# Performance work log

Measured on AMD Instinct MI355X. Metric: run time of the kernel, lower is better.

Reference implementation:

```python
import jax, jax.numpy as jnp
import numpy as np

N_EXPERTS = 8
D_MODEL = 1024
D_FF = 2048
NUM_TOKENS = 16384


def setup_inputs() -> dict:
    key = jax.random.key(0)
    k1, k2, k3, k4 = jax.random.split(key, 4)
    x = jax.random.normal(k1, (NUM_TOKENS, D_MODEL), dtype=jnp.float32)
    expert_indices = jax.random.randint(k2, (NUM_TOKENS,), 0, N_EXPERTS, dtype=jnp.int32)
    # init per nn.init.normal_(std=0.02)
    gate_up_weight = 0.02 * jax.random.normal(k3, (N_EXPERTS, 2 * D_FF, D_MODEL), dtype=jnp.float32)
    down_weight = 0.02 * jax.random.normal(k4, (N_EXPERTS, D_MODEL, D_FF), dtype=jnp.float32)
    return {"x": x, "expert_indices": expert_indices,
            "gate_up_weight": gate_up_weight, "down_weight": down_weight}


def reference(x, expert_indices, gate_up_weight, down_weight):
    # Faithful math: each token t uses expert e = expert_indices[t]:
    #   combined = x @ gate_up_weight[e].T ; gate, up = split ; h = silu(gate)*up
    #   out = h @ down_weight[e].T
    # Implemented as a fixed loop over the (small) expert set with masked
    # accumulation, avoiding the original's per-token [2F,D] weight gather.
    n_experts = gate_up_weight.shape[0]
    d_ff = down_weight.shape[2]
    out = jnp.zeros((x.shape[0], down_weight.shape[1]), dtype=x.dtype)
    for e in range(n_experts):
        combined = x @ gate_up_weight[e].T                  # [T, 2*d_ff]
        gate, up = combined[:, :d_ff], combined[:, d_ff:]
        hidden = jax.nn.silu(gate) * up                     # [T, d_ff]
        o = hidden @ down_weight[e].T                       # [T, d_model]
        out = out + jnp.where((expert_indices == e)[:, None], o, 0.0)
    return out
```

## Files before the change

### kernel.cpp

```cpp
#include <hip/hip_runtime.h>

#define NTOK 16384
#define DM 1024
#define DFF 2048
#define NE 8

typedef unsigned short u16;
typedef __attribute__((ext_vector_type(8))) short bf16x8;
typedef __attribute__((ext_vector_type(4))) float f32x4;

__device__ __forceinline__ u16 f2bf(float f) {
  unsigned u = __float_as_uint(f);
  u += 0x7fff + ((u >> 16) & 1);
  return (u16)(u >> 16);
}

__device__ __forceinline__ void async16(const void* g, void* l) {
  __builtin_amdgcn_global_load_lds(
      (const __attribute__((address_space(1))) unsigned int*)g,
      (__attribute__((address_space(3))) unsigned int*)l, 16, 0, 0);
}

__global__ void k_count(const int* __restrict__ idx, int* __restrict__ counts) {
  int t = blockIdx.x * 256 + threadIdx.x;
  atomicAdd(&counts[idx[t]], 1);
}

__global__ void k_offsets(int* __restrict__ c) {
  if (threadIdx.x == 0) {
    int acc = 0;
    for (int e = 0; e < NE; e++) { c[8 + e] = acc; c[16 + e] = acc; acc += c[e]; }
  }
}

__global__ void k_scatter(const int* __restrict__ idx, int* __restrict__ cursor,
                          int* __restrict__ tl) {
  int t = blockIdx.x * 256 + threadIdx.x;
  int pos = atomicAdd(&cursor[idx[t]], 1);
  tl[pos] = t;
}

__global__ void k_cvt_xw(const float* __restrict__ x, const float* __restrict__ wgu,
                         u16* __restrict__ xb, u16* __restrict__ wgub) {
  const size_t N1 = (size_t)NTOK * DM;
  const size_t N2 = (size_t)NE * 2 * DFF * DM;
  const size_t total4 = (N1 + N2) / 4;
  for (size_t q = (size_t)blockIdx.x * 256 + threadIdx.x; q < total4;
       q += (size_t)gridDim.x * 256) {
    size_t i = q * 4;
    const float* s;
    u16* d;
    if (i < N1) { s = x + i; d = xb + i; }
    else { s = wgu + (i - N1); d = wgub + (i - N1); }
    float4 v = *(const float4*)s;
    ushort4 o;
    o.x = f2bf(v.x); o.y = f2bf(v.y); o.z = f2bf(v.z); o.w = f2bf(v.w);
    *(ushort4*)d = o;
  }
}

__global__ __launch_bounds__(512, 2) void k_gemm1(
    const u16* __restrict__ xb, const u16* __restrict__ wgu,
    u16* __restrict__ hid, const int* __restrict__ tl,
    const int* __restrict__ offs, const int* __restrict__ counts,
    const float* __restrict__ wd, u16* __restrict__ wdb) {
  int wg = blockIdx.x;
  int tid = threadIdx.x;

  {
    const size_t WD4 = (size_t)NE * DM * DFF / 4;
    for (size_t i = (size_t)wg * 512 + tid; i < WD4; i += (size_t)1152 * 512) {
      float4 v = *(const float4*)(wd + i * 4);
      ushort4 o;
      o.x = f2bf(v.x); o.y = f2bf(v.y); o.z = f2bf(v.z); o.w = f2bf(v.w);
      *(ushort4*)(wdb + i * 4) = o;
    }
  }

  int e = wg & 7;
  int r = wg >> 3;
  int bx = r % 9;
  int by = r / 9;
  int Me = counts[e];
  int m0 = bx * 256;
  if (m0 >= Me) return;
  int n0 = by * 128;
  int oe = offs[e];
  const int* tle = tl + oe;

  int lane = tid & 63;
  int wid = tid >> 6;
  int wm = wid >> 2;
  int wn = wid & 3;

  __shared__ u16 lds[2][2][256 * 64];

  int lr = lane >> 3;
  int swz = ((lane & 7) ^ lr) * 8;
  const u16* pA[4];
  const u16* pB[4];
#pragma unroll
  for (int j = 0; j < 4; j++) {
    int c = j * 8 + wid;
    int a = m0 + c * 8 + lr;
    if (a >= Me) a = Me - 1;
    pA[j] = xb + (size_t)tle[a] * DM + swz;
    int b = c * 8 + lr;
    int grow = ((b >> 5) & 1) * DFF + n0 + ((b >> 6) & 3) * 32 + (b & 31);
    pB[j] = wgu + ((size_t)e * 2 * DFF + grow) * DM + swz;
  }

  f32x4 acc[8][4];
#pragma unroll
  for (int m = 0; m < 8; m++)
#pragma unroll
    for (int f = 0; f < 4; f++) acc[m][f] = (f32x4){0.f, 0.f, 0.f, 0.f};

  const int r15 = lane & 15;
  const int hi4 = lane >> 4;
  const int rx = r15 & 7;

#pragma unroll
  for (int j = 0; j < 4; j++) {
    int off = (j * 8 + wid) * 1024;
    async16(pA[j], (char*)&lds[0][0][0] + off);
    async16(pB[j], (char*)&lds[0][1][0] + off);
  }
  asm volatile("s_waitcnt vmcnt(0)" ::: "memory");
  __builtin_amdgcn_s_barrier();
  __builtin_amdgcn_sched_barrier(0);

  int cur = 0;
#pragma unroll 1
  for (int t = 0; t < DM / 64; t++) {
    const char* Ab = (const char*)&lds[cur][0][0];
    const char* Bb = (const char*)&lds[cur][1][0];
    char* LA = (char*)&lds[cur ^ 1][0][0];
    char* LB = (char*)&lds[cur ^ 1][1][0];
    int k1 = (t + 1) * 64;
    bool pf = (t < DM / 64 - 1);
    bf16x8 bfr[4][2];
#pragma unroll
    for (int p = 0; p < 4; p++) {
      if (p == 0) {
#pragma unroll
        for (int f = 0; f < 4; f++)
#pragma unroll
          for (int kk = 0; kk < 2; kk++) {
            int row = wn * 64 + f * 16 + r15;
            bfr[f][kk] = *(const bf16x8*)(Bb + row * 128 + (((kk * 4 + hi4) ^ rx) * 16));
          }
      }
      bf16x8 af[2][2];
#pragma unroll
      for (int i = 0; i < 2; i++)
#pragma unroll
        for (int kk = 0; kk < 2; kk++) {
          int row = wm * 128 + (2 * p + i) * 16 + r15;
          af[i][kk] = *(const bf16x8*)(Ab + row * 128 + (((kk * 4 + hi4) ^ rx) * 16));
        }
      if (pf && p < 2) {
#pragma unroll
        for (int j = 0; j < 2; j++) {
          int jj = p * 2 + j;
          int off = (jj * 8 + wid) * 1024;
          async16(pA[jj] + k1, LA + off);
          async16(pB[jj] + k1, LB + off);
        }
      }
      __builtin_amdgcn_sched_barrier(0);
      __builtin_amdgcn_s_setprio(1);
#pragma unroll
      for (int kk = 0; kk < 2; kk++)
#pragma unroll
        for (int i = 0; i < 2; i++)
#pragma unroll
          for (int f = 0; f < 4; f++)
            acc[2 * p + i][f] = __builtin_amdgcn_mfma_f32_16x16x32_bf16(
                af[i][kk], bfr[f][kk], acc[2 * p + i][f], 0, 0, 0);
      __builtin_amdgcn_s_setprio(0);
      __builtin_amdgcn_sched_barrier(0);
    }
    asm volatile("s_waitcnt vmcnt(0)" ::: "memory");
    __builtin_amdgcn_s_barrier();
    __builtin_amdgcn_sched_barrier(0);
    cur ^= 1;
  }

  int colb = n0 + wn * 32 + r15;
#pragma unroll
  for (int m = 0; m < 8; m++) {
#pragma unroll
    for (int rr = 0; rr < 4; rr++) {
      int gm = m0 + wm * 128 + m * 16 + hi4 * 4 + rr;
      if (gm < Me) {
        size_t rowp = (size_t)(oe + gm) * DFF;
#pragma unroll
        for (int f = 0; f < 2; f++) {
          float g = acc[m][f][rr];
          float u = acc[m][f + 2][rr];
          float s = g / (1.0f + __expf(-g));
          hid[rowp + colb + f * 16] = f2bf(s * u);
        }
      }
    }
  }
}

__global__ __launch_bounds__(512, 2) void k_gemm2(
    const u16* __restrict__ hid, const u16* __restrict__ wd,
    float* __restrict__ out, const int* __restrict__ tl,
    const int* __restrict__ offs, const int* __restrict__ counts) {
  int wg = blockIdx.x;
  int e = wg & 7;
  int r = wg >> 3;
  int bx = r % 9;
  int by = r / 9;
  int Me = counts[e];
  int m0 = bx * 256;
  if (m0 >= Me) return;
  int n0 = by * 256;
  int oe = offs[e];
  const int* tle = tl + oe;

  int tid = threadIdx.x;
  int lane = tid & 63;
  int wid = tid >> 6;
  int wm = wid >> 2;
  int wn = wid & 3;

  __shared__ u16 lds[2][2][256 * 64];

  int lr = lane >> 3;
  int swz = ((lane & 7) ^ lr) * 8;
  const u16* pA[4];
  const u16* pB[4];
#pragma unroll
  for (int j = 0; j < 4; j++) {
    int c = j * 8 + wid;
    int a = m0 + c * 8 + lr;
    if (a >= Me) a = Me - 1;
    pA[j] = hid + (size_t)(oe + a) * DFF + swz;
    pB[j] = wd + ((size_t)e * DM + n0 + c * 8 + lr) * DFF + swz;
  }

  f32x4 acc[8][4];
#pragma unroll
  for (int m = 0; m < 8; m++)
#pragma unroll
    for (int f = 0; f < 4; f++) acc[m][f] = (f32x4){0.f, 0.f, 0.f, 0.f};

  const int r15 = lane & 15;
  const int hi4 = lane >> 4;
  const int rx = r15 & 7;

#pragma unroll
  for (int j = 0; j < 4; j++) {
    int off = (j * 8 + wid) * 1024;
    async16(pA[j], (char*)&lds[0][0][0] + off);
    async16(pB[j], (char*)&lds[0][1][0] + off);
  }
  asm volatile("s_waitcnt vmcnt(0)" ::: "memory");
  __builtin_amdgcn_s_barrier();
  __builtin_amdgcn_sched_barrier(0);

  int cur = 0;
#pragma unroll 1
  for (int t = 0; t < DFF / 64; t++) {
    const char* Ab = (const char*)&lds[cur][0][0];
    const char* Bb = (const char*)&lds[cur][1][0];
    char* LA = (char*)&lds[cur ^ 1][0][0];
    char* LB = (char*)&lds[cur ^ 1][1][0];
    int k1 = (t + 1) * 64;
    bool pf = (t < DFF / 64 - 1);
    bf16x8 bfr[4][2];
#pragma unroll
    for (int p = 0; p < 4; p++) {
      if (p == 0) {
#pragma unroll
        for (int f = 0; f < 4; f++)
#pragma unroll
          for (int kk = 0; kk < 2; kk++) {
            int row = wn * 64 + f * 16 + r15;
            bfr[f][kk] = *(const bf16x8*)(Bb + row * 128 + (((kk * 4 + hi4) ^ rx) * 16));
          }
      }
      bf16x8 af[2][2];
#pragma unroll
      for (int i = 0; i < 2; i++)
#pragma unroll
        for (int kk = 0; kk < 2; kk++) {
          int row = wm * 128 + (2 * p + i) * 16 + r15;
          af[i][kk] = *(const bf16x8*)(Ab + row * 128 + (((kk * 4 + hi4) ^ rx) * 16));
        }
      if (pf && p < 2) {
#pragma unroll
        for (int j = 0; j < 2; j++) {
          int jj = p * 2 + j;
          int off = (jj * 8 + wid) * 1024;
          async16(pA[jj] + k1, LA + off);
          async16(pB[jj] + k1, LB + off);
        }
      }
      __builtin_amdgcn_sched_barrier(0);
      __builtin_amdgcn_s_setprio(1);
#pragma unroll
      for (int kk = 0; kk < 2; kk++)
#pragma unroll
        for (int i = 0; i < 2; i++)
#pragma unroll
          for (int f = 0; f < 4; f++)
            acc[2 * p + i][f] = __builtin_amdgcn_mfma_f32_16x16x32_bf16(
                af[i][kk], bfr[f][kk], acc[2 * p + i][f], 0, 0, 0);
      __builtin_amdgcn_s_setprio(0);
      __builtin_amdgcn_sched_barrier(0);
    }
    asm volatile("s_waitcnt vmcnt(0)" ::: "memory");
    __builtin_amdgcn_s_barrier();
    __builtin_amdgcn_sched_barrier(0);
    cur ^= 1;
  }

  int colb = n0 + wn * 64 + r15;
#pragma unroll
  for (int m = 0; m < 8; m++) {
#pragma unroll
    for (int rr = 0; rr < 4; rr++) {
      int gm = m0 + wm * 128 + m * 16 + hi4 * 4 + rr;
      if (gm < Me) {
        int tk = tle[gm];
#pragma unroll
        for (int f = 0; f < 4; f++)
          out[(size_t)tk * DM + colb + f * 16] = acc[m][f][rr];
      }
    }
  }
}

extern "C" void kernel_launch(void* const* d_in, const int* in_sizes, int n_in,
                              void* d_out, int out_size, void* d_ws, size_t ws_size,
                              hipStream_t stream) {
  const float* x   = (const float*)d_in[0];
  const int* eidx  = (const int*)d_in[1];
  const float* wgu = (const float*)d_in[2];
  const float* wd  = (const float*)d_in[3];
  float* out = (float*)d_out;
  char* ws = (char*)d_ws;

  int* ctrl = (int*)ws;
  int* toklist = (int*)(ws + 256);
  u16* xb   = (u16*)(ws + 65792);
  u16* wgub = (u16*)(ws + 65792 + 33554432ull);
  u16* wdb  = (u16*)(ws + 65792 + 33554432ull + 67108864ull);
  u16* hid  = (u16*)(ws + 65792 + 33554432ull + 67108864ull + 33554432ull);

  hipMemsetAsync(ws, 0, 256, stream);
  k_count<<<NTOK / 256, 256, 0, stream>>>(eidx, ctrl);
  k_offsets<<<1, 64, 0, stream>>>(ctrl);
  k_scatter<<<NTOK / 256, 256, 0, stream>>>(eidx, ctrl + 16, toklist);

  k_cvt_xw<<<2048, 256, 0, stream>>>(x, wgu, xb, wgub);

  k_gemm1<<<9 * 16 * NE, 512, 0, stream>>>(xb, wgub, hid, toklist, ctrl + 8, ctrl, wd, wdb);
  k_gemm2<<<9 * 4 * NE, 512, 0, stream>>>(hid, wdb, out, toklist, ctrl + 8, ctrl);
}
```

Before: 465.6 us.

## Interleave down-weight conversion into gemm1 main loop and halve gemm2 N-tile

Rather than converting the fp32 down-projection weights to bf16 in a prologue before the GEMM, each gemm1 workgroup now spreads its eight conversion chunks over the first eight K-iterations, loading in the first phase and storing in the third so the memory traffic overlaps with MFMA work. Workgroups with no tokens convert their chunks directly and then exit. Separately, gemm2 switches from 256x256 to 256x128 tiles and doubles its grid, giving more workgroups to fill the CUs and shrinking LDS and accumulator use. The risks are extra register pressure and stalls in gemm1's inner loop, plus more A-tile re-reads in gemm2.

```diff
diff --git a/kernel.cpp b/kernel.cpp
--- a/kernel.cpp
+++ b/kernel.cpp
@@ -66,16 +66,9 @@
     const float* __restrict__ wd, u16* __restrict__ wdb) {
   int wg = blockIdx.x;
   int tid = threadIdx.x;
-
-  {
-    const size_t WD4 = (size_t)NE * DM * DFF / 4;
-    for (size_t i = (size_t)wg * 512 + tid; i < WD4; i += (size_t)1152 * 512) {
-      float4 v = *(const float4*)(wd + i * 4);
-      ushort4 o;
-      o.x = f2bf(v.x); o.y = f2bf(v.y); o.z = f2bf(v.z); o.w = f2bf(v.w);
-      *(ushort4*)(wdb + i * 4) = o;
-    }
-  }
+  const size_t WD4 = (size_t)NE * DM * DFF / 4;
+  const size_t FSTRIDE = (size_t)1152 * 512;
+  size_t fbase = (size_t)wg * 512 + tid;
 
   int e = wg & 7;
   int r = wg >> 3;
@@ -83,7 +76,18 @@
   int by = r / 9;
   int Me = counts[e];
   int m0 = bx * 256;
-  if (m0 >= Me) return;
+  if (m0 >= Me) {
+    for (int c = 0; c < 8; c++) {
+      size_t i = fbase + (size_t)c * FSTRIDE;
+      if (i < WD4) {
+        float4 v = *(const float4*)(wd + i * 4);
+        ushort4 o;
+        o.x = f2bf(v.x); o.y = f2bf(v.y); o.z = f2bf(v.z); o.w = f2bf(v.w);
+        *(ushort4*)(wdb + i * 4) = o;
+      }
+    }
+    return;
+  }
   int n0 = by * 128;
   int oe = offs[e];
   const int* tle = tl + oe;
@@ -139,6 +143,9 @@
     char* LB = (char*)&lds[cur ^ 1][1][0];
     int k1 = (t + 1) * 64;
     bool pf = (t < DM / 64 - 1);
+    size_t fi = fbase + (size_t)t * FSTRIDE;
+    bool dofold = (t < 8) && (fi < WD4);
+    float4 fv;
     bf16x8 bfr[4][2];
 #pragma unroll
     for (int p = 0; p < 4; p++) {
@@ -150,6 +157,7 @@
             int row = wn * 64 + f * 16 + r15;
             bfr[f][kk] = *(const bf16x8*)(Bb + row * 128 + (((kk * 4 + hi4) ^ rx) * 16));
           }
+        if (dofold) fv = *(const float4*)(wd + fi * 4);
       }
       bf16x8 af[2][2];
 #pragma unroll
@@ -167,6 +175,11 @@
           async16(pA[jj] + k1, LA + off);
           async16(pB[jj] + k1, LB + off);
         }
+      }
+      if (p == 2 && dofold) {
+        ushort4 o;
+        o.x = f2bf(fv.x); o.y = f2bf(fv.y); o.z = f2bf(fv.z); o.w = f2bf(fv.w);
+        *(ushort4*)(wdb + fi * 4) = o;
       }
       __builtin_amdgcn_sched_barrier(0);
       __builtin_amdgcn_s_setprio(1);
@@ -219,7 +232,7 @@
   int Me = counts[e];
   int m0 = bx * 256;
   if (m0 >= Me) return;
-  int n0 = by * 256;
+  int n0 = by * 128;
   int oe = offs[e];
   const int* tle = tl + oe;
 
@@ -229,37 +242,42 @@
   int wm = wid >> 2;
   int wn = wid & 3;
 
-  __shared__ u16 lds[2][2][256 * 64];
+  __shared__ u16 ldsA[2][256 * 64];
+  __shared__ u16 ldsB[2][128 * 64];
 
   int lr = lane >> 3;
   int swz = ((lane & 7) ^ lr) * 8;
   const u16* pA[4];
-  const u16* pB[4];
+  const u16* pB[2];
 #pragma unroll
   for (int j = 0; j < 4; j++) {
     int c = j * 8 + wid;
     int a = m0 + c * 8 + lr;
     if (a >= Me) a = Me - 1;
     pA[j] = hid + (size_t)(oe + a) * DFF + swz;
+  }
+#pragma unroll
+  for (int j = 0; j < 2; j++) {
+    int c = j * 8 + wid;
     pB[j] = wd + ((size_t)e * DM + n0 + c * 8 + lr) * DFF + swz;
   }
 
-  f32x4 acc[8][4];
+  f32x4 acc[8][2];
 #pragma unroll
   for (int m = 0; m < 8; m++)
 #pragma unroll
-    for (int f = 0; f < 4; f++) acc[m][f] = (f32x4){0.f, 0.f, 0.f, 0.f};
+    for (int f = 0; f < 2; f++) acc[m][f] = (f32x4){0.f, 0.f, 0.f, 0.f};
 
   const int r15 = lane & 15;
   const int hi4 = lane >> 4;
   const int rx = r15 & 7;
 
 #pragma unroll
-  for (int j = 0; j < 4; j++) {
-    int off = (j * 8 + wid) * 1024;
-    async16(pA[j], (char*)&lds[0][0][0] + off);
-    async16(pB[j], (char*)&lds[0][1][0] + off);
-  }
+  for (int j = 0; j < 4; j++)
+    async16(pA[j], (char*)&ldsA[0][0] + (j * 8 + wid) * 1024);
+#pragma unroll
+  for (int j = 0; j < 2; j++)
+    async16(pB[j], (char*)&ldsB[0][0] + (j * 8 + wid) * 1024);
   asm volatile("s_waitcnt vmcnt(0)" ::: "memory");
   __builtin_amdgcn_s_barrier();
   __builtin_amdgcn_sched_barrier(0);
@@ -267,51 +285,50 @@
   int cur = 0;
 #pragma unroll 1
   for (int t = 0; t < DFF / 64; t++) {
-    const char* Ab = (const char*)&lds[cur][0][0];
-    const char* Bb = (const char*)&lds[cur][1][0];
-    char* LA = (char*)&lds[cur ^ 1][0][0];
-    char* LB = (char*)&lds[cur ^ 1][1][0];
+    const char* Ab = (const char*)&ldsA[cur][0];
+    const char* Bb = (const char*)&ldsB[cur][0];
+    char* LA = (char*)&ldsA[cur ^ 1][0];
+    char* LB = (char*)&ldsB[cur ^ 1][0];
     int k1 = (t + 1) * 64;
     bool pf = (t < DFF / 64 - 1);
-    bf16x8 bfr[4][2];
-#pragma unroll
-    for (int p = 0; p < 4; p++) {
+    bf16x8 bfr[2][2];
+#pragma unroll
+    for (int p = 0; p < 2; p++) {
       if (p == 0) {
 #pragma unroll
-        for (int f = 0; f < 4; f++)
+        for (int f = 0; f < 2; f++)
 #pragma unroll
           for (int kk = 0; kk < 2; kk++) {
-            int row = wn * 64 + f * 16 + r15;
+            int row = wn * 32 + f * 16 + r15;
             bfr[f][kk] = *(const bf16x8*)(Bb + row * 128 + (((kk * 4 + hi4) ^ rx) * 16));
           }
       }
-      bf16x8 af[2][2];
-#pragma unroll
-      for (int i = 0; i < 2; i++)
+      bf16x8 af[4][2];
+#pragma unroll
+      for (int i = 0; i < 4; i++)
 #pragma unroll
         for (int kk = 0; kk < 2; kk++) {
-          int row = wm * 128 + (2 * p + i) * 16 + r15;
+          int row = wm * 128 + (p * 4 + i) * 16 + r15;
           af[i][kk] = *(const bf16x8*)(Ab + row * 128 + (((kk * 4 + hi4) ^ rx) * 16));
         }
-      if (pf && p < 2) {
+      if (pf) {
 #pragma unroll
         for (int j = 0; j < 2; j++) {
           int jj = p * 2 + j;
-          int off = (jj * 8 + wid) * 1024;
-          async16(pA[jj] + k1, LA + off);
-          async16(pB[jj] + k1, LB + off);
-        }
+          async16(pA[jj] + k1, LA + (jj * 8 + wid) * 1024);
+        }
+        async16(pB[p] + k1, LB + (p * 8 + wid) * 1024);
       }
       __builtin_amdgcn_sched_barrier(0);
       __builtin_amdgcn_s_setprio(1);
 #pragma unroll
       for (int kk = 0; kk < 2; kk++)
 #pragma unroll
-        for (int i = 0; i < 2; i++)
-#pragma unroll
-          for (int f = 0; f < 4; f++)
-            acc[2 * p + i][f] = __builtin_amdgcn_mfma_f32_16x16x32_bf16(
-                af[i][kk], bfr[f][kk], acc[2 * p + i][f], 0, 0, 0);
+        for (int i = 0; i < 4; i++)
+#pragma unroll
+          for (int f = 0; f < 2; f++)
+            acc[p * 4 + i][f] = __builtin_amdgcn_mfma_f32_16x16x32_bf16(
+                af[i][kk], bfr[f][kk], acc[p * 4 + i][f], 0, 0, 0);
       __builtin_amdgcn_s_setprio(0);
       __builtin_amdgcn_sched_barrier(0);
     }
@@ -321,7 +338,7 @@
     cur ^= 1;
   }
 
-  int colb = n0 + wn * 64 + r15;
+  int colb = n0 + wn * 32 + r15;
 #pragma unroll
   for (int m = 0; m < 8; m++) {
 #pragma unroll
@@ -330,7 +347,7 @@
       if (gm < Me) {
         int tk = tle[gm];
 #pragma unroll
-        for (int f = 0; f < 4; f++)
+        for (int f = 0; f < 2; f++)
           out[(size_t)tk * DM + colb + f * 16] = acc[m][f][rr];
       }
     }
@@ -362,5 +379,5 @@
   k_cvt_xw<<<2048, 256, 0, stream>>>(x, wgu, xb, wgub);
 
   k_gemm1<<<9 * 16 * NE, 512, 0, stream>>>(xb, wgub, hid, toklist, ctrl + 8, ctrl, wd, wdb);
-  k_gemm2<<<9 * 4 * NE, 512, 0, stream>>>(hid, wdb, out, toklist, ctrl + 8, ctrl);
-}
+  k_gemm2<<<9 * 8 * NE, 512, 0, stream>>>(hid, wdb, out, toklist, ctrl + 8, ctrl);
+}
```

After: 479.4 us. 1.03x slower.

## Split gemm2 tail rows into a separate small-tile overflow kernel

Applied to the files above, without the earlier changes.

The down-projection GEMM now launches only eight 256-row M tiles per expert. A new kernel with 64-row tiles handles the rows beyond 2048 for experts whose token count exceeds that. This avoids a mostly-empty ninth full-size tile that extended the grid beyond one wave and wasted compute. It adds a kernel launch and assumes no expert has more than 2304 tokens.

```diff
diff --git a/kernel.cpp b/kernel.cpp
--- a/kernel.cpp
+++ b/kernel.cpp
@@ -214,8 +214,8 @@
   int wg = blockIdx.x;
   int e = wg & 7;
   int r = wg >> 3;
-  int bx = r % 9;
-  int by = r / 9;
+  int bx = r & 7;
+  int by = r >> 3;
   int Me = counts[e];
   int m0 = bx * 256;
   if (m0 >= Me) return;
@@ -337,6 +337,130 @@
   }
 }
 
+__global__ __launch_bounds__(512, 2) void k_gemm2_ovf(
+    const u16* __restrict__ hid, const u16* __restrict__ wd,
+    float* __restrict__ out, const int* __restrict__ tl,
+    const int* __restrict__ offs, const int* __restrict__ counts) {
+  int wg = blockIdx.x;
+  int e = wg & 7;
+  int r = wg >> 3;
+  int bx = r & 3;
+  int by = r >> 2;
+  int Me = counts[e];
+  int m0 = 2048 + bx * 64;
+  if (m0 >= Me) return;
+  int n0 = by * 256;
+  int oe = offs[e];
+  const int* tle = tl + oe;
+
+  int tid = threadIdx.x;
+  int lane = tid & 63;
+  int wid = tid >> 6;
+  int wm = wid >> 2;
+  int wn = wid & 3;
+
+  __shared__ u16 ldsA[2][64 * 64];
+  __shared__ u16 ldsB[2][256 * 64];
+
+  int lr = lane >> 3;
+  int swz = ((lane & 7) ^ lr) * 8;
+  const u16* pAo;
+  const u16* pB[4];
+  {
+    int a = m0 + wid * 8 + lr;
+    if (a >= Me) a = Me - 1;
+    pAo = hid + (size_t)(oe + a) * DFF + swz;
+  }
+#pragma unroll
+  for (int j = 0; j < 4; j++) {
+    int c = j * 8 + wid;
+    pB[j] = wd + ((size_t)e * DM + n0 + c * 8 + lr) * DFF + swz;
+  }
+
+  f32x4 acc[2][4];
+#pragma unroll
+  for (int m = 0; m < 2; m++)
+#pragma unroll
+    for (int f = 0; f < 4; f++) acc[m][f] = (f32x4){0.f, 0.f, 0.f, 0.f};
+
+  const int r15 = lane & 15;
+  const int hi4 = lane >> 4;
+  const int rx = r15 & 7;
+
+  async16(pAo, (char*)&ldsA[0][0] + wid * 1024);
+#pragma unroll
+  for (int j = 0; j < 4; j++)
+    async16(pB[j], (char*)&ldsB[0][0] + (j * 8 + wid) * 1024);
+  asm volatile("s_waitcnt vmcnt(0)" ::: "memory");
+  __builtin_amdgcn_s_barrier();
+  __builtin_amdgcn_sched_barrier(0);
+
+  int cur = 0;
+#pragma unroll 1
+  for (int t = 0; t < DFF / 64; t++) {
+    const char* Ab = (const char*)&ldsA[cur][0];
+    const char* Bb = (const char*)&ldsB[cur][0];
+    char* LA = (char*)&ldsA[cur ^ 1][0];
+    char* LB = (char*)&ldsB[cur ^ 1][0];
+    int k1 = (t + 1) * 64;
+    bool pf = (t < DFF / 64 - 1);
+#pragma unroll
+    for (int kk = 0; kk < 2; kk++) {
+      bf16x8 bfr[4], af[2];
+#pragma unroll
+      for (int f = 0; f < 4; f++) {
+        int row = wn * 64 + f * 16 + r15;
+        bfr[f] = *(const bf16x8*)(Bb + row * 128 + (((kk * 4 + hi4) ^ rx) * 16));
+      }
+#pragma unroll
+      for (int i = 0; i < 2; i++) {
+        int row = wm * 32 + i * 16 + r15;
+        af[i] = *(const bf16x8*)(Ab + row * 128 + (((kk * 4 + hi4) ^ rx) * 16));
+      }
+      if (pf) {
+        if (kk == 0) {
+          async16(pAo + k1, LA + wid * 1024);
+#pragma unroll
+          for (int j = 0; j < 2; j++)
+            async16(pB[j] + k1, LB + (j * 8 + wid) * 1024);
+        } else {
+#pragma unroll
+          for (int j = 2; j < 4; j++)
+            async16(pB[j] + k1, LB + (j * 8 + wid) * 1024);
+        }
+      }
+      __builtin_amdgcn_sched_barrier(0);
+      __builtin_amdgcn_s_setprio(1);
+#pragma unroll
+      for (int i = 0; i < 2; i++)
+#pragma unroll
+        for (int f = 0; f < 4; f++)
+          acc[i][f] = __builtin_amdgcn_mfma_f32_16x16x32_bf16(af[i], bfr[f], acc[i][f], 0, 0, 0);
+      __builtin_amdgcn_s_setprio(0);
+      __builtin_amdgcn_sched_barrier(0);
+    }
+    asm volatile("s_waitcnt vmcnt(0)" ::: "memory");
+    __builtin_amdgcn_s_barrier();
+    __builtin_amdgcn_sched_barrier(0);
+    cur ^= 1;
+  }
+
+  int colb = n0 + wn * 64 + r15;
+#pragma unroll
+  for (int m = 0; m < 2; m++) {
+#pragma unroll
+    for (int rr = 0; rr < 4; rr++) {
+      int gm = m0 + wm * 32 + m * 16 + hi4 * 4 + rr;
+      if (gm < Me) {
+        int tk = tle[gm];
+#pragma unroll
+        for (int f = 0; f < 4; f++)
+          out[(size_t)tk * DM + colb + f * 16] = acc[m][f][rr];
+      }
+    }
+  }
+}
+
 extern "C" void kernel_launch(void* const* d_in, const int* in_sizes, int n_in,
                               void* d_out, int out_size, void* d_ws, size_t ws_size,
                               hipStream_t stream) {
@@ -362,5 +486,6 @@
   k_cvt_xw<<<2048, 256, 0, stream>>>(x, wgu, xb, wgub);
 
   k_gemm1<<<9 * 16 * NE, 512, 0, stream>>>(xb, wgub, hid, toklist, ctrl + 8, ctrl, wd, wdb);
-  k_gemm2<<<9 * 4 * NE, 512, 0, stream>>>(hid, wdb, out, toklist, ctrl + 8, ctrl);
-}
+  k_gemm2<<<8 * 4 * NE, 512, 0, stream>>>(hid, wdb, out, toklist, ctrl + 8, ctrl);
+  k_gemm2_ovf<<<4 * 4 * NE, 512, 0, stream>>>(hid, wdb, out, toklist, ctrl + 8, ctrl);
+}
```

After: 465.6 us (median of 2 runs). Within noise of the previous version (-0.0%).
